# Kernel tuning notes

Measured on AMD Instinct MI355X. Metric: run time of the kernel, lower is better.

Reference implementation:

```python
import jax, jax.numpy as jnp
import numpy as np

EMB = 1024
HEADS = 16
EPS = 1e-6


def setup_inputs() -> dict:
    key = jax.random.key(0)
    ks = jax.random.split(key, 12)
    B, S, D = 2, 2048, EMB
    scale = 1.0 / np.sqrt(D)
    inp = {
        "v": jax.random.normal(ks[0], (B, S, D), jnp.float32),
        "k": jax.random.normal(ks[1], (B, S, D), jnp.float32),
        "q": jax.random.normal(ks[2], (B, S, D), jnp.float32),
        "Wv": jax.random.normal(ks[3], (D, D), jnp.float32) * scale,
        "bv": jnp.zeros((D,), jnp.float32),
        "Wk": jax.random.normal(ks[4], (D, D), jnp.float32) * scale,
        "bk": jnp.zeros((D,), jnp.float32),
        "Wq": jax.random.normal(ks[5], (D, D), jnp.float32) * scale,
        "bq": jnp.zeros((D,), jnp.float32),
        "Wo": jax.random.normal(ks[6], (D, D), jnp.float32) * scale,
        "bo": jnp.zeros((D,), jnp.float32),
        "gamma": jnp.ones((D,), jnp.float32),
        "beta": jnp.zeros((D,), jnp.float32),
    }
    return inp


def reference(v, k, q, Wv, bv, Wk, bk, Wq, bq, Wo, bo, gamma, beta):
    B, S, D = q.shape
    H = HEADS
    d = D // H  # head depth

    def split_heads(x):  # [B,S,D] -> [B,H,S,d]
        return x.reshape(B, S, H, d).transpose(0, 2, 1, 3)

    V = split_heads(v @ Wv + bv)
    K = split_heads(k @ Wk + bk)
    Q = split_heads(q @ Wq + bq)

    # scaled dot-product attention (full score matrix, no mask)
    scores = jnp.einsum("bhqd,bhkd->bhqk", Q, K) / jnp.sqrt(jnp.float32(d))
    attn = jax.nn.softmax(scores, axis=-1)
    ctx = jnp.einsum("bhqk,bhkd->bhqd", attn, V)

    ctx = ctx.transpose(0, 2, 1, 3).reshape(B, S, D)
    out = ctx @ Wo + bo + q  # final dense + residual

    # LayerNormalization(epsilon=1e-6) over last axis
    mu = jnp.mean(out, axis=-1, keepdims=True)
    var = jnp.var(out, axis=-1, keepdims=True)
    return gamma * (out - mu) * jax.lax.rsqrt(var + EPS) + beta
```

## Files before the change

### kernel.cpp

```cpp
#include <hip/hip_runtime.h>
#include <hip/hip_bf16.h>
#include <math.h>

#define D_EMB 1024
#define NBATCH 2
#define SEQ 2048
#define NH 16
#define HDIM 64
#define MTOT (NBATCH*SEQ)
#define NT (SEQ/64)

typedef unsigned short u16;
typedef __attribute__((ext_vector_type(8))) short bf16x8;
typedef __attribute__((ext_vector_type(4))) float f32x4;
typedef __attribute__((ext_vector_type(16))) float f32x16;
typedef __attribute__((ext_vector_type(4))) unsigned short u16x4;
typedef __attribute__((ext_vector_type(4))) unsigned int u32x4;

__device__ __forceinline__ u16 f2b(float f) {
  union { float f; unsigned u; } x; x.f = f;
  unsigned r = x.u + 0x7fffu + ((x.u >> 16) & 1u);
  return (u16)(r >> 16);
}

__device__ __forceinline__ void gld_lds16(const u16* g, u16* l) {
  __builtin_amdgcn_global_load_lds(
      (const __attribute__((address_space(1))) void*)g,
      (__attribute__((address_space(3))) void*)l, 16, 0, 0);
}

__global__ __launch_bounds__(256) void convert_qkv(
    const float* __restrict__ v, const float* __restrict__ k, const float* __restrict__ q,
    u16* __restrict__ vb, u16* __restrict__ kb, u16* __restrict__ qb) {
  int idx = blockIdx.x * 256 + threadIdx.x;
  float4 a;
  u16x4 o;
  a = ((const float4*)v)[idx];
  o.x = f2b(a.x); o.y = f2b(a.y); o.z = f2b(a.z); o.w = f2b(a.w);
  ((u16x4*)vb)[idx] = o;
  a = ((const float4*)k)[idx];
  o.x = f2b(a.x); o.y = f2b(a.y); o.z = f2b(a.z); o.w = f2b(a.w);
  ((u16x4*)kb)[idx] = o;
  a = ((const float4*)q)[idx];
  o.x = f2b(a.x); o.y = f2b(a.y); o.z = f2b(a.z); o.w = f2b(a.w);
  ((u16x4*)qb)[idx] = o;
}

__global__ __launch_bounds__(256) void transpose_w(
    const float* __restrict__ Wv, const float* __restrict__ Wk,
    const float* __restrict__ Wq, const float* __restrict__ Wo,
    u16* __restrict__ Wvt, u16* __restrict__ Wkt,
    u16* __restrict__ Wqt, u16* __restrict__ Wot) {
  __shared__ float tile[32][33];
  int z = blockIdx.z;
  const float* W = (z==0) ? Wv : (z==1) ? Wk : (z==2) ? Wq : Wo;
  u16* Wt = (z==0) ? Wvt : (z==1) ? Wkt : (z==2) ? Wqt : Wot;
  int tx = threadIdx.x, ty = threadIdx.y;
  int n0 = blockIdx.x * 32, k0 = blockIdx.y * 32;
#pragma unroll
  for (int i = 0; i < 4; ++i)
    tile[ty + i*8][tx] = W[(size_t)(k0 + ty + i*8) * D_EMB + n0 + tx];
  __syncthreads();
#pragma unroll
  for (int i = 0; i < 4; ++i)
    Wt[(size_t)(n0 + ty + i*8) * D_EMB + k0 + tx] = f2b(tile[tx][ty + i*8]);
}

__global__ __launch_bounds__(256) void transpose_v(
    const u16* __restrict__ Vh, u16* __restrict__ Vt) {
  __shared__ u16 t[64][65];
  const int bhx = blockIdx.y, s0 = blockIdx.x * 64;
  const int tid = threadIdx.x;
  const u16* src = Vh + ((size_t)bhx * SEQ + s0) * HDIM;
  const int r = tid >> 3, seg = (tid & 7) * 8;
  bf16x8 a0 = *(const bf16x8*)(src + (size_t)r * HDIM + seg);
  bf16x8 a1 = *(const bf16x8*)(src + (size_t)(r + 32) * HDIM + seg);
#pragma unroll
  for (int j = 0; j < 8; ++j) {
    t[r][seg + j] = (u16)a0[j];
    t[r + 32][seg + j] = (u16)a1[j];
  }
  __syncthreads();
  const int dd = tid >> 3, ss = (tid & 7) * 8;
  bf16x8 w0, w1;
#pragma unroll
  for (int j = 0; j < 8; ++j) {
    w0[j] = (short)t[ss + j][dd];
    w1[j] = (short)t[ss + j][dd + 32];
  }
  *(bf16x8*)(Vt + ((size_t)bhx * HDIM + dd) * SEQ + s0 + ss) = w0;
  *(bf16x8*)(Vt + ((size_t)bhx * HDIM + dd + 32) * SEQ + s0 + ss) = w1;
}

__device__ __forceinline__ void gemm_loop(
    const u16* __restrict__ A, const u16* __restrict__ Bt,
    u16* lds_a, u16* lds_b, int bm, int bn, int wid, int lane,
    int wr, int wc, f32x4 acc[4][4]) {
#pragma unroll 1
  for (int kt = 0; kt < D_EMB/64; ++kt) {
    __syncthreads();
#pragma unroll
    for (int i = 0; i < 4; ++i) {
      int chunk = i*4 + wid;
      int row = chunk*8 + (lane >> 3);
      int slot = (lane & 7) ^ (row & 7);
      const u16* srcA = A + (size_t)(bm*128 + row) * D_EMB + kt*64 + slot*8;
      gld_lds16(srcA, lds_a + chunk*512);
      const u16* srcB = Bt + (size_t)(bn*128 + row) * D_EMB + kt*64 + slot*8;
      gld_lds16(srcB, lds_b + chunk*512);
    }
    __syncthreads();
#pragma unroll
    for (int st = 0; st < 2; ++st) {
      bf16x8 af[4], bfr[4];
#pragma unroll
      for (int mb = 0; mb < 4; ++mb) {
        int row = wr*64 + mb*16 + (lane & 15);
        int slot = (st*4 + (lane >> 4)) ^ (row & 7);
        af[mb] = *(const bf16x8*)(lds_a + row*64 + slot*8);
      }
#pragma unroll
      for (int nb = 0; nb < 4; ++nb) {
        int row = wc*64 + nb*16 + (lane & 15);
        int slot = (st*4 + (lane >> 4)) ^ (row & 7);
        bfr[nb] = *(const bf16x8*)(lds_b + row*64 + slot*8);
      }
#pragma unroll
      for (int mb = 0; mb < 4; ++mb)
#pragma unroll
        for (int nb = 0; nb < 4; ++nb)
          acc[mb][nb] = __builtin_amdgcn_mfma_f32_16x16x32_bf16(af[mb], bfr[nb], acc[mb][nb], 0, 0, 0);
    }
  }
}

__global__ __launch_bounds__(256) void gemm_qkv(
    const u16* __restrict__ vb, const u16* __restrict__ kb, const u16* __restrict__ qb,
    const u16* __restrict__ Wvt, const u16* __restrict__ Wkt, const u16* __restrict__ Wqt,
    const float* __restrict__ bv, const float* __restrict__ bk, const float* __restrict__ bq,
    u16* __restrict__ Vh, u16* __restrict__ Kh, u16* __restrict__ Qh) {
  __shared__ u16 lds_a[128*64];
  __shared__ u16 lds_b[128*64];
  int z = blockIdx.z;
  const u16* A  = (z==0) ? vb : (z==1) ? kb : qb;
  const u16* Bt = (z==0) ? Wvt : (z==1) ? Wkt : Wqt;
  const float* bias = (z==0) ? bv : (z==1) ? bk : bq;
  u16* Out = (z==0) ? Vh : (z==1) ? Kh : Qh;
  int tid = threadIdx.x, wid = tid >> 6, lane = tid & 63;
  int wr = wid >> 1, wc = wid & 1;
  int bm = blockIdx.y, bn = blockIdx.x;
  f32x4 acc[4][4];
#pragma unroll
  for (int i = 0; i < 4; ++i)
#pragma unroll
    for (int j = 0; j < 4; ++j) acc[i][j] = (f32x4){0.f,0.f,0.f,0.f};
  gemm_loop(A, Bt, lds_a, lds_b, bm, bn, wid, lane, wr, wc, acc);
  int g = lane >> 4, c = lane & 15;
  const float scl = (z == 2) ? 0.18033688f : 1.0f;
#pragma unroll
  for (int mb = 0; mb < 4; ++mb) {
    int row0 = bm*128 + wr*64 + mb*16 + g*4;
#pragma unroll
    for (int nb = 0; nb < 4; ++nb) {
      int col = bn*128 + wc*64 + nb*16 + c;
      float bsv = bias[col];
      int h = col >> 6, dd = col & 63;
#pragma unroll
      for (int r = 0; r < 4; ++r) {
        int m = row0 + r; int b = m >> 11, s = m & (SEQ-1);
        Out[(((size_t)b*NH + h)*SEQ + s)*HDIM + dd] = f2b((acc[mb][nb][r] + bsv) * scl);
      }
    }
  }
}

__global__ __launch_bounds__(256, 2) void attn_k(
    const u16* __restrict__ Qh, const u16* __restrict__ Kh,
    const u16* __restrict__ Vt, u16* __restrict__ ctx) {
  __shared__ u16 kt_lds[2][64*64];
  __shared__ u16 vt_lds[2][64*64];
  const int tid = threadIdx.x, wid = tid >> 6, lane = tid & 63;
  const int lo5 = lane & 31, hi = lane >> 5;
  const int bid = blockIdx.x;
  const int xcd = bid & 7, idx = bid >> 3;
  const int qblk = idx & 15, bhg = idx >> 4;
  const int bh = bhg * 8 + xcd;
  const int qb = qblk * 128 + wid * 32;
  const size_t base = (size_t)bh * SEQ * HDIM;

  const int srow = tid >> 3;
  const int c0 = (tid & 7) ^ (srow & 7) ^ (srow >> 3);
  const int c1 = c0 ^ 4;
  const u16* kp0 = Kh + base + (size_t)srow * HDIM + c0*8;
  const u16* kp1 = Kh + base + (size_t)(srow+32) * HDIM + c1*8;
  const u16* vp0 = Vt + base + (size_t)srow * SEQ + c0*8;
  const u16* vp1 = Vt + base + (size_t)(srow+32) * SEQ + c1*8;

  const int r7 = lo5 & 7, r3 = lo5 >> 3;
  int offs0[4], offs1[4];
#pragma unroll
  for (int t = 0; t < 4; ++t) {
    int p = (2*t + hi) ^ r7 ^ r3;
    offs0[t] = lo5*128 + p*16;
    offs1[t] = (lo5+32)*128 + (p^4)*16;
  }
  const char* ktbase = (const char*)&kt_lds[0][0];
  const char* vtbase = (const char*)&vt_lds[0][0];

  bf16x8 qf[4];
#pragma unroll
  for (int t = 0; t < 4; ++t)
    qf[t] = *(const bf16x8*)(Qh + base + (size_t)(qb + lo5)*HDIM + t*16 + hi*8);

  f32x16 z16;
#pragma unroll
  for (int i = 0; i < 16; ++i) z16[i] = 0.f;

  f32x16 o0, o1;
#pragma unroll
  for (int i = 0; i < 16; ++i) { o0[i] = 0.f; o1[i] = 0.f; }
  float lsum = 0.f;

#define STAGE(B) do { \
    gld_lds16(kp0, &kt_lds[B][wid*512]); \
    gld_lds16(kp1, &kt_lds[B][2048 + wid*512]); \
    gld_lds16(vp0, &vt_lds[B][wid*512]); \
    gld_lds16(vp1, &vt_lds[B][2048 + wid*512]); \
    kp0 += 64*HDIM; kp1 += 64*HDIM; vp0 += 64; vp1 += 64; \
  } while (0)

#define TILE(B, VMSTR, DOSTAGE) do { \
    asm volatile("s_waitcnt " VMSTR ::: "memory"); \
    __builtin_amdgcn_sched_barrier(0); \
    __builtin_amdgcn_s_barrier();             \
    __builtin_amdgcn_sched_barrier(0); \
    const char* kb_ = ktbase + (B)*8192; \
    const char* vb_ = vtbase + (B)*8192; \
    bf16x8 kf0[4], kf1[4], vf0[4], vf1[4]; \
    _Pragma("unroll") for (int t = 0; t < 4; ++t) { \
      kf0[t] = *(const bf16x8*)(kb_ + offs0[t]); \
      kf1[t] = *(const bf16x8*)(kb_ + offs1[t]); \
      vf0[t] = *(const bf16x8*)(vb_ + offs0[t]); \
      vf1[t] = *(const bf16x8*)(vb_ + offs1[t]); } \
    asm volatile("s_waitcnt lgkmcnt(0)" ::: "memory"); \
    __builtin_amdgcn_sched_barrier(0); \
    __builtin_amdgcn_s_barrier();             \
    __builtin_amdgcn_sched_barrier(0); \
    if (DOSTAGE) { STAGE(B); } \
    __builtin_amdgcn_sched_barrier(0); \
    __builtin_amdgcn_s_setprio(1); \
    f32x16 st0 = __builtin_amdgcn_mfma_f32_32x32x16_bf16(kf0[0], qf[0], z16, 0, 0, 0); \
    f32x16 st1 = __builtin_amdgcn_mfma_f32_32x32x16_bf16(kf1[0], qf[0], z16, 0, 0, 0); \
    _Pragma("unroll") for (int t = 1; t < 4; ++t) { \
      st0 = __builtin_amdgcn_mfma_f32_32x32x16_bf16(kf0[t], qf[t], st0, 0, 0, 0); \
      st1 = __builtin_amdgcn_mfma_f32_32x32x16_bf16(kf1[t], qf[t], st1, 0, 0, 0); } \
    __builtin_amdgcn_s_setprio(0); \
    _Pragma("unroll") for (int r = 0; r < 16; ++r) { \
      st0[r] = exp2f(st0[r]); st1[r] = exp2f(st1[r]); } \
    float ps = st0[0] + st0[1]; \
    _Pragma("unroll") for (int r = 2; r < 16; ++r) ps += st0[r]; \
    _Pragma("unroll") for (int r = 0; r < 16; ++r) ps += st1[r]; \
    lsum += ps; \
    bf16x8 pa[4]; \
    _Pragma("unroll") for (int ks = 0; ks < 2; ++ks) { \
      const f32x16& s_ = ks ? st1 : st0; \
      unsigned X[8]; \
      _Pragma("unroll") for (int w = 0; w < 8; ++w) { \
        float lo_f = s_[2*w], hi_f = s_[2*w + 1]; \
        asm("v_cvt_pk_bf16_f32 %0, %1, %2" : "=v"(X[w]) : "v"(lo_f), "v"(hi_f)); } \
      asm volatile("v_permlane32_swap_b32 %0, %1" : "+v"(X[0]), "+v"(X[2])); \
      asm volatile("v_permlane32_swap_b32 %0, %1" : "+v"(X[1]), "+v"(X[3])); \
      asm volatile("v_permlane32_swap_b32 %0, %1" : "+v"(X[4]), "+v"(X[6])); \
      asm volatile("v_permlane32_swap_b32 %0, %1" : "+v"(X[5]), "+v"(X[7])); \
      union { u32x4 u; bf16x8 b; } cva, cvb; \
      cva.u = (u32x4){X[0], X[1], X[2], X[3]}; \
      cvb.u = (u32x4){X[4], X[5], X[6], X[7]}; \
      pa[2*ks]   = cva.b; \
      pa[2*ks+1] = cvb.b; } \
    __builtin_amdgcn_s_setprio(1); \
    _Pragma("unroll") for (int t = 0; t < 4; ++t) { \
      o0 = __builtin_amdgcn_mfma_f32_32x32x16_bf16(pa[t], vf0[t], o0, 0, 0, 0); \
      o1 = __builtin_amdgcn_mfma_f32_32x32x16_bf16(pa[t], vf1[t], o1, 0, 0, 0); } \
    __builtin_amdgcn_s_setprio(0); \
  } while (0)

  STAGE(0);
  STAGE(1);

#pragma unroll 1
  for (int kv = 0; kv < NT - 2; kv += 2) {
    TILE(0, "vmcnt(4)", 1);
    TILE(1, "vmcnt(4)", 1);
  }
  TILE(0, "vmcnt(4)", 0);
  TILE(1, "vmcnt(0)", 0);

#undef STAGE
#undef TILE

  lsum += __shfl_xor(lsum, 32);
  float linv = 1.0f / lsum;
  const int b = bh >> 4, h = bh & 15;
#pragma unroll
  for (int r = 0; r < 16; ++r) {
    int crow = (r & 3) + 8*(r >> 2) + 4*hi;
    float lr = __int_as_float(
        __builtin_amdgcn_ds_bpermute(crow << 2, __float_as_int(linv)));
    int s = qb + crow;
    u16* row = ctx + ((size_t)(b*SEQ + s))*D_EMB + h*64;
    row[lo5]      = f2b(o0[r] * lr);
    row[32 + lo5] = f2b(o1[r] * lr);
  }
}

__global__ __launch_bounds__(256) void gemm_out(
    const u16* __restrict__ ctx, const u16* __restrict__ Wot,
    const float* __restrict__ bo, const float* __restrict__ resid,
    float* __restrict__ preln) {
  __shared__ u16 lds_a[128*64];
  __shared__ u16 lds_b[128*64];
  int tid = threadIdx.x, wid = tid >> 6, lane = tid & 63;
  int wr = wid >> 1, wc = wid & 1;
  int bm = blockIdx.y, bn = blockIdx.x;
  f32x4 acc[4][4];
#pragma unroll
  for (int i = 0; i < 4; ++i)
#pragma unroll
    for (int j = 0; j < 4; ++j) acc[i][j] = (f32x4){0.f,0.f,0.f,0.f};
  gemm_loop(ctx, Wot, lds_a, lds_b, bm, bn, wid, lane, wr, wc, acc);
  int g = lane >> 4, c = lane & 15;
#pragma unroll
  for (int mb = 0; mb < 4; ++mb) {
    int row0 = bm*128 + wr*64 + mb*16 + g*4;
#pragma unroll
    for (int nb = 0; nb < 4; ++nb) {
      int col = bn*128 + wc*64 + nb*16 + c;
      float bsv = bo[col];
#pragma unroll
      for (int r = 0; r < 4; ++r) {
        int m = row0 + r;
        preln[(size_t)m*D_EMB + col] = acc[mb][nb][r] + bsv + resid[(size_t)m*D_EMB + col];
      }
    }
  }
}

__global__ __launch_bounds__(256) void ln_k(
    const float* __restrict__ preln, const float* __restrict__ gamma,
    const float* __restrict__ beta, float* __restrict__ out) {
  int row = blockIdx.x, tid = threadIdx.x;
  float4 x = ((const float4*)(preln + (size_t)row*D_EMB))[tid];
  float s  = x.x + x.y + x.z + x.w;
  float ss = x.x*x.x + x.y*x.y + x.z*x.z + x.w*x.w;
#pragma unroll
  for (int off = 32; off; off >>= 1) {
    s  += __shfl_xor(s, off);
    ss += __shfl_xor(ss, off);
  }
  __shared__ float red_s[4], red_ss[4];
  int wid = tid >> 6, lane = tid & 63;
  if (lane == 0) { red_s[wid] = s; red_ss[wid] = ss; }
  __syncthreads();
  s  = red_s[0] + red_s[1] + red_s[2] + red_s[3];
  ss = red_ss[0] + red_ss[1] + red_ss[2] + red_ss[3];
  float mu = s * (1.0f/1024.0f);
  float var = ss * (1.0f/1024.0f) - mu*mu;
  float rstd = rsqrtf(var + 1e-6f);
  float4 gm = ((const float4*)gamma)[tid];
  float4 bt = ((const float4*)beta)[tid];
  float4 y;
  y.x = (x.x - mu)*rstd*gm.x + bt.x;
  y.y = (x.y - mu)*rstd*gm.y + bt.y;
  y.z = (x.z - mu)*rstd*gm.z + bt.z;
  y.w = (x.w - mu)*rstd*gm.w + bt.w;
  ((float4*)(out + (size_t)row*D_EMB))[tid] = y;
}

extern "C" void kernel_launch(void* const* d_in, const int* in_sizes, int n_in,
                              void* d_out, int out_size, void* d_ws, size_t ws_size,
                              hipStream_t stream) {
  const float* v_in  = (const float*)d_in[0];
  const float* k_in  = (const float*)d_in[1];
  const float* q_in  = (const float*)d_in[2];
  const float* Wv    = (const float*)d_in[3];
  const float* bv    = (const float*)d_in[4];
  const float* Wk    = (const float*)d_in[5];
  const float* bk    = (const float*)d_in[6];
  const float* Wq    = (const float*)d_in[7];
  const float* bq    = (const float*)d_in[8];
  const float* Wo    = (const float*)d_in[9];
  const float* bo    = (const float*)d_in[10];
  const float* gamma = (const float*)d_in[11];
  const float* beta  = (const float*)d_in[12];
  char* ws = (char*)d_ws;

  const size_t TOKB = (size_t)MTOT * D_EMB * 2;
  const size_t WB   = (size_t)D_EMB * D_EMB * 2;
  size_t o_qb = 0;
  size_t o_kb = o_qb + TOKB;
  size_t o_vb = o_kb + TOKB;
  size_t o_wq = o_vb + TOKB;
  size_t o_wk = o_wq + WB;
  size_t o_wv = o_wk + WB;
  size_t o_wo = o_wv + WB;
  size_t o_Qh = o_wo + WB;
  size_t o_Kh = o_Qh + TOKB;
  size_t o_Vt = o_Kh + TOKB;
  size_t o_cx = o_Vt + TOKB;

  u16* qb  = (u16*)(ws + o_qb);
  u16* kb  = (u16*)(ws + o_kb);
  u16* vb  = (u16*)(ws + o_vb);
  u16* wqt = (u16*)(ws + o_wq);
  u16* wkt = (u16*)(ws + o_wk);
  u16* wvt = (u16*)(ws + o_wv);
  u16* wot = (u16*)(ws + o_wo);
  u16* Qh  = (u16*)(ws + o_Qh);
  u16* Kh  = (u16*)(ws + o_Kh);
  u16* Vt  = (u16*)(ws + o_Vt);
  u16* cx  = (u16*)(ws + o_cx);
  u16* Vh  = cx;
  float* preln = (float*)(ws + 0);

  convert_qkv<<<4096, 256, 0, stream>>>(v_in, k_in, q_in, vb, kb, qb);
  transpose_w<<<dim3(32, 32, 4), dim3(32, 8), 0, stream>>>(Wv, Wk, Wq, Wo, wvt, wkt, wqt, wot);
  gemm_qkv<<<dim3(8, 32, 3), 256, 0, stream>>>(vb, kb, qb, wvt, wkt, wqt, bv, bk, bq, Vh, Kh, Qh);
  transpose_v<<<dim3(32, 32), 256, 0, stream>>>(Vh, Vt);
  attn_k<<<512, 256, 0, stream>>>(Qh, Kh, Vt, cx);
  gemm_out<<<dim3(8, 32), 256, 0, stream>>>(cx, wot, bo, q_in, preln);
  ln_k<<<4096, 256, 0, stream>>>(preln, gamma, beta, (float*)d_out);
}
```

Before: 154.9 us.

## Split attention KV loop across two wave groups per block and merge via LDS

Doubles the attention block to 512 threads. Two groups of four waves each process half of the key/value sequence for the same query tile, using separate LDS double buffers. The second group then writes its partial outputs and row sums to LDS, and the first group adds them before normalising and storing. This halves the serial KV loop per wave and raises waves per CU, at the cost of an extra LDS reduction and a tighter register budget from the launch bounds.

```diff
diff --git a/kernel.cpp b/kernel.cpp
--- a/kernel.cpp
+++ b/kernel.cpp
@@ -8,7 +8,7 @@
 #define NH 16
 #define HDIM 64
 #define MTOT (NBATCH*SEQ)
-#define NT (SEQ/64)
+#define NTS 16
 
 typedef unsigned short u16;
 typedef __attribute__((ext_vector_type(8))) short bf16x8;
@@ -174,27 +174,29 @@
   }
 }
 
-__global__ __launch_bounds__(256, 2) void attn_k(
+__global__ __launch_bounds__(512, 4) void attn_k(
     const u16* __restrict__ Qh, const u16* __restrict__ Kh,
     const u16* __restrict__ Vt, u16* __restrict__ ctx) {
-  __shared__ u16 kt_lds[2][64*64];
-  __shared__ u16 vt_lds[2][64*64];
+  __shared__ u16 kt_lds[2][2][64*64];
+  __shared__ u16 vt_lds[2][2][64*64];
   const int tid = threadIdx.x, wid = tid >> 6, lane = tid & 63;
+  const int grp = wid >> 2, wlocal = wid & 3;
   const int lo5 = lane & 31, hi = lane >> 5;
   const int bid = blockIdx.x;
   const int xcd = bid & 7, idx = bid >> 3;
   const int qblk = idx & 15, bhg = idx >> 4;
   const int bh = bhg * 8 + xcd;
-  const int qb = qblk * 128 + wid * 32;
+  const int qb = qblk * 128 + wlocal * 32;
   const size_t base = (size_t)bh * SEQ * HDIM;
 
-  const int srow = tid >> 3;
-  const int c0 = (tid & 7) ^ (srow & 7) ^ (srow >> 3);
+  const int stid = tid & 255;
+  const int srow = stid >> 3;
+  const int c0 = (stid & 7) ^ (srow & 7) ^ (srow >> 3);
   const int c1 = c0 ^ 4;
-  const u16* kp0 = Kh + base + (size_t)srow * HDIM + c0*8;
-  const u16* kp1 = Kh + base + (size_t)(srow+32) * HDIM + c1*8;
-  const u16* vp0 = Vt + base + (size_t)srow * SEQ + c0*8;
-  const u16* vp1 = Vt + base + (size_t)(srow+32) * SEQ + c1*8;
+  const u16* kp0 = Kh + base + (size_t)(grp*1024 + srow) * HDIM + c0*8;
+  const u16* kp1 = Kh + base + (size_t)(grp*1024 + srow + 32) * HDIM + c1*8;
+  const u16* vp0 = Vt + base + (size_t)srow * SEQ + grp*1024 + c0*8;
+  const u16* vp1 = Vt + base + (size_t)(srow+32) * SEQ + grp*1024 + c1*8;
 
   const int r7 = lo5 & 7, r3 = lo5 >> 3;
   int offs0[4], offs1[4];
@@ -204,8 +206,8 @@
     offs0[t] = lo5*128 + p*16;
     offs1[t] = (lo5+32)*128 + (p^4)*16;
   }
-  const char* ktbase = (const char*)&kt_lds[0][0];
-  const char* vtbase = (const char*)&vt_lds[0][0];
+  const char* ktb = (const char*)&kt_lds[grp][0][0];
+  const char* vtb = (const char*)&vt_lds[grp][0][0];
 
   bf16x8 qf[4];
 #pragma unroll
@@ -222,10 +224,10 @@
   float lsum = 0.f;
 
 #define STAGE(B) do { \
-    gld_lds16(kp0, &kt_lds[B][wid*512]); \
-    gld_lds16(kp1, &kt_lds[B][2048 + wid*512]); \
-    gld_lds16(vp0, &vt_lds[B][wid*512]); \
-    gld_lds16(vp1, &vt_lds[B][2048 + wid*512]); \
+    gld_lds16(kp0, &kt_lds[grp][B][wlocal*512]); \
+    gld_lds16(kp1, &kt_lds[grp][B][2048 + wlocal*512]); \
+    gld_lds16(vp0, &vt_lds[grp][B][wlocal*512]); \
+    gld_lds16(vp1, &vt_lds[grp][B][2048 + wlocal*512]); \
     kp0 += 64*HDIM; kp1 += 64*HDIM; vp0 += 64; vp1 += 64; \
   } while (0)
 
@@ -234,8 +236,8 @@
     __builtin_amdgcn_sched_barrier(0); \
     __builtin_amdgcn_s_barrier();             \
     __builtin_amdgcn_sched_barrier(0); \
-    const char* kb_ = ktbase + (B)*8192; \
-    const char* vb_ = vtbase + (B)*8192; \
+    const char* kb_ = ktb + (B)*8192; \
+    const char* vb_ = vtb + (B)*8192; \
     bf16x8 kf0[4], kf1[4], vf0[4], vf1[4]; \
     _Pragma("unroll") for (int t = 0; t < 4; ++t) { \
       kf0[t] = *(const bf16x8*)(kb_ + offs0[t]); \
@@ -288,7 +290,7 @@
   STAGE(1);
 
 #pragma unroll 1
-  for (int kv = 0; kv < NT - 2; kv += 2) {
+  for (int kv = 0; kv < NTS - 2; kv += 2) {
     TILE(0, "vmcnt(4)", 1);
     TILE(1, "vmcnt(4)", 1);
   }
@@ -299,17 +301,34 @@
 #undef TILE
 
   lsum += __shfl_xor(lsum, 32);
-  float linv = 1.0f / lsum;
-  const int b = bh >> 4, h = bh & 15;
-#pragma unroll
-  for (int r = 0; r < 16; ++r) {
-    int crow = (r & 3) + 8*(r >> 2) + 4*hi;
-    float lr = __int_as_float(
-        __builtin_amdgcn_ds_bpermute(crow << 2, __float_as_int(linv)));
-    int s = qb + crow;
-    u16* row = ctx + ((size_t)(b*SEQ + s))*D_EMB + h*64;
-    row[lo5]      = f2b(o0[r] * lr);
-    row[32 + lo5] = f2b(o1[r] * lr);
+  float* ox0 = (float*)&kt_lds[0][0][0];
+  float* ox1 = (float*)&vt_lds[0][0][0];
+  float* lx  = ox1 + 4*1088;
+  if (grp == 1) {
+    float* d0 = ox0 + wlocal*1088 + lane*17;
+    float* d1 = ox1 + wlocal*1088 + lane*17;
+#pragma unroll
+    for (int i = 0; i < 16; ++i) { d0[i] = o0[i]; d1[i] = o1[i]; }
+    if (hi == 0) lx[wlocal*32 + lo5] = lsum;
+  }
+  __syncthreads();
+  if (grp == 0) {
+    const float* s0 = ox0 + wlocal*1088 + lane*17;
+    const float* s1 = ox1 + wlocal*1088 + lane*17;
+#pragma unroll
+    for (int i = 0; i < 16; ++i) { o0[i] += s0[i]; o1[i] += s1[i]; }
+    float linv = 1.0f / (lsum + lx[wlocal*32 + lo5]);
+    const int b = bh >> 4, h = bh & 15;
+#pragma unroll
+    for (int r = 0; r < 16; ++r) {
+      int crow = (r & 3) + 8*(r >> 2) + 4*hi;
+      float lr = __int_as_float(
+          __builtin_amdgcn_ds_bpermute(crow << 2, __float_as_int(linv)));
+      int s = qb + crow;
+      u16* row = ctx + ((size_t)(b*SEQ + s))*D_EMB + h*64;
+      row[lo5]      = f2b(o0[r] * lr);
+      row[32 + lo5] = f2b(o1[r] * lr);
+    }
   }
 }
 
@@ -426,7 +445,7 @@
   transpose_w<<<dim3(32, 32, 4), dim3(32, 8), 0, stream>>>(Wv, Wk, Wq, Wo, wvt, wkt, wqt, wot);
   gemm_qkv<<<dim3(8, 32, 3), 256, 0, stream>>>(vb, kb, qb, wvt, wkt, wqt, bv, bk, bq, Vh, Kh, Qh);
   transpose_v<<<dim3(32, 32), 256, 0, stream>>>(Vh, Vt);
-  attn_k<<<512, 256, 0, stream>>>(Qh, Kh, Vt, cx);
+  attn_k<<<512, 512, 0, stream>>>(Qh, Kh, Vt, cx);
   gemm_out<<<dim3(8, 32), 256, 0, stream>>>(cx, wot, bo, q_in, preln);
   ln_k<<<4096, 256, 0, stream>>>(preln, gamma, beta, (float*)d_out);
 }
```

Measured after the change: 321.9 us. +107.7%, slower.

## Quad-buffer attention K/V tiles and use bf16 residual and pre-LN buffers

Applied to the files above, without the earlier changes.

The attention kernel moves from two LDS stages to four, so each tile's prefetch targets a buffer two tiles ahead. This removes the second workgroup barrier and lgkmcnt wait that used to guard buffer reuse inside every tile. Separately, the output GEMM now reads the bf16 copy of q as the residual and writes the pre-LayerNorm activations as bf16 into a reused workspace buffer, halving that traffic. The trade-off is double the LDS per block, which may lower occupancy, plus precision loss in the residual and the pre-LN values.

```diff
diff --git a/kernel.cpp b/kernel.cpp
--- a/kernel.cpp
+++ b/kernel.cpp
@@ -21,6 +21,10 @@
   union { float f; unsigned u; } x; x.f = f;
   unsigned r = x.u + 0x7fffu + ((x.u >> 16) & 1u);
   return (u16)(r >> 16);
+}
+__device__ __forceinline__ float b2f(u16 u) {
+  union { unsigned u; float f; } x; x.u = ((unsigned)u) << 16;
+  return x.f;
 }
 
 __device__ __forceinline__ void gld_lds16(const u16* g, u16* l) {
@@ -177,8 +181,8 @@
 __global__ __launch_bounds__(256, 2) void attn_k(
     const u16* __restrict__ Qh, const u16* __restrict__ Kh,
     const u16* __restrict__ Vt, u16* __restrict__ ctx) {
-  __shared__ u16 kt_lds[2][64*64];
-  __shared__ u16 vt_lds[2][64*64];
+  __shared__ u16 kt_lds[4][64*64];
+  __shared__ u16 vt_lds[4][64*64];
   const int tid = threadIdx.x, wid = tid >> 6, lane = tid & 63;
   const int lo5 = lane & 31, hi = lane >> 5;
   const int bid = blockIdx.x;
@@ -229,7 +233,7 @@
     kp0 += 64*HDIM; kp1 += 64*HDIM; vp0 += 64; vp1 += 64; \
   } while (0)
 
-#define TILE(B, VMSTR, DOSTAGE) do { \
+#define TILE(B, VMSTR, DOSTAGE, SB) do { \
     asm volatile("s_waitcnt " VMSTR ::: "memory"); \
     __builtin_amdgcn_sched_barrier(0); \
     __builtin_amdgcn_s_barrier();             \
@@ -242,11 +246,7 @@
       kf1[t] = *(const bf16x8*)(kb_ + offs1[t]); \
       vf0[t] = *(const bf16x8*)(vb_ + offs0[t]); \
       vf1[t] = *(const bf16x8*)(vb_ + offs1[t]); } \
-    asm volatile("s_waitcnt lgkmcnt(0)" ::: "memory"); \
-    __builtin_amdgcn_sched_barrier(0); \
-    __builtin_amdgcn_s_barrier();             \
-    __builtin_amdgcn_sched_barrier(0); \
-    if (DOSTAGE) { STAGE(B); } \
+    if (DOSTAGE) { STAGE(SB); } \
     __builtin_amdgcn_sched_barrier(0); \
     __builtin_amdgcn_s_setprio(1); \
     f32x16 st0 = __builtin_amdgcn_mfma_f32_32x32x16_bf16(kf0[0], qf[0], z16, 0, 0, 0); \
@@ -288,12 +288,16 @@
   STAGE(1);
 
 #pragma unroll 1
-  for (int kv = 0; kv < NT - 2; kv += 2) {
-    TILE(0, "vmcnt(4)", 1);
-    TILE(1, "vmcnt(4)", 1);
-  }
-  TILE(0, "vmcnt(4)", 0);
-  TILE(1, "vmcnt(0)", 0);
+  for (int kv = 0; kv < NT - 4; kv += 4) {
+    TILE(0, "vmcnt(4)", 1, 2);
+    TILE(1, "vmcnt(4)", 1, 3);
+    TILE(2, "vmcnt(4)", 1, 0);
+    TILE(3, "vmcnt(4)", 1, 1);
+  }
+  TILE(0, "vmcnt(4)", 1, 2);
+  TILE(1, "vmcnt(4)", 1, 3);
+  TILE(2, "vmcnt(4)", 0, 0);
+  TILE(3, "vmcnt(0)", 0, 0);
 
 #undef STAGE
 #undef TILE
@@ -315,8 +319,8 @@
 
 __global__ __launch_bounds__(256) void gemm_out(
     const u16* __restrict__ ctx, const u16* __restrict__ Wot,
-    const float* __restrict__ bo, const float* __restrict__ resid,
-    float* __restrict__ preln) {
+    const float* __restrict__ bo, const u16* __restrict__ resid,
+    u16* __restrict__ preln) {
   __shared__ u16 lds_a[128*64];
   __shared__ u16 lds_b[128*64];
   int tid = threadIdx.x, wid = tid >> 6, lane = tid & 63;
@@ -339,19 +343,21 @@
 #pragma unroll
       for (int r = 0; r < 4; ++r) {
         int m = row0 + r;
-        preln[(size_t)m*D_EMB + col] = acc[mb][nb][r] + bsv + resid[(size_t)m*D_EMB + col];
+        float v = acc[mb][nb][r] + bsv + b2f(resid[(size_t)m*D_EMB + col]);
+        preln[(size_t)m*D_EMB + col] = f2b(v);
       }
     }
   }
 }
 
 __global__ __launch_bounds__(256) void ln_k(
-    const float* __restrict__ preln, const float* __restrict__ gamma,
+    const u16* __restrict__ preln, const float* __restrict__ gamma,
     const float* __restrict__ beta, float* __restrict__ out) {
   int row = blockIdx.x, tid = threadIdx.x;
-  float4 x = ((const float4*)(preln + (size_t)row*D_EMB))[tid];
-  float s  = x.x + x.y + x.z + x.w;
-  float ss = x.x*x.x + x.y*x.y + x.z*x.z + x.w*x.w;
+  u16x4 xr = ((const u16x4*)(preln + (size_t)row*D_EMB))[tid];
+  float x0 = b2f(xr.x), x1 = b2f(xr.y), x2 = b2f(xr.z), x3 = b2f(xr.w);
+  float s  = x0 + x1 + x2 + x3;
+  float ss = x0*x0 + x1*x1 + x2*x2 + x3*x3;
 #pragma unroll
   for (int off = 32; off; off >>= 1) {
     s  += __shfl_xor(s, off);
@@ -369,10 +375,10 @@
   float4 gm = ((const float4*)gamma)[tid];
   float4 bt = ((const float4*)beta)[tid];
   float4 y;
-  y.x = (x.x - mu)*rstd*gm.x + bt.x;
-  y.y = (x.y - mu)*rstd*gm.y + bt.y;
-  y.z = (x.z - mu)*rstd*gm.z + bt.z;
-  y.w = (x.w - mu)*rstd*gm.w + bt.w;
+  y.x = (x0 - mu)*rstd*gm.x + bt.x;
+  y.y = (x1 - mu)*rstd*gm.y + bt.y;
+  y.z = (x2 - mu)*rstd*gm.z + bt.z;
+  y.w = (x3 - mu)*rstd*gm.w + bt.w;
   ((float4*)(out + (size_t)row*D_EMB))[tid] = y;
 }
 
@@ -420,13 +426,13 @@
   u16* Vt  = (u16*)(ws + o_Vt);
   u16* cx  = (u16*)(ws + o_cx);
   u16* Vh  = cx;
-  float* preln = (float*)(ws + 0);
+  u16* preln = vb;
 
   convert_qkv<<<4096, 256, 0, stream>>>(v_in, k_in, q_in, vb, kb, qb);
   transpose_w<<<dim3(32, 32, 4), dim3(32, 8), 0, stream>>>(Wv, Wk, Wq, Wo, wvt, wkt, wqt, wot);
   gemm_qkv<<<dim3(8, 32, 3), 256, 0, stream>>>(vb, kb, qb, wvt, wkt, wqt, bv, bk, bq, Vh, Kh, Qh);
   transpose_v<<<dim3(32, 32), 256, 0, stream>>>(Vh, Vt);
   attn_k<<<512, 256, 0, stream>>>(Qh, Kh, Vt, cx);
-  gemm_out<<<dim3(8, 32), 256, 0, stream>>>(cx, wot, bo, q_in, preln);
+  gemm_out<<<dim3(8, 32), 256, 0, stream>>>(cx, wot, bo, qb, preln);
   ln_k<<<4096, 256, 0, stream>>>(preln, gamma, beta, (float*)d_out);
 }
```

After: 155.4 us. About the same (+0.3%).
